# Kernel optimization log

Measured on AMD Instinct MI355X. Metric: run time of the kernel, lower is better.

## Reference

```python
import jax, jax.numpy as jnp
import numpy as np

BETA = 0.25
NUM_CODES = 512      # K
CODE_DIM = 64        # D (codebook_size)
N_TOKENS = 131072    # N


def setup_inputs() -> dict:
    key = jax.random.key(0)
    kx, kc = jax.random.split(key)
    x = jax.random.normal(kx, (N_TOKENS, CODE_DIM), dtype=jnp.float32)
    # keras 'random_uniform' initializer: U(-0.05, 0.05)
    codebook = jax.random.uniform(kc, (NUM_CODES, CODE_DIM), dtype=jnp.float32,
                                  minval=-0.05, maxval=0.05)
    return {"x": x, "codebook": codebook}


def reference(x, codebook):
    # Squared Euclidean distances [N, K] via expansion; argmin is identical
    # to argmin of tf.norm (sqrt is monotone).
    x2 = jnp.sum(x * x, axis=-1, keepdims=True)            # [N, 1]
    c2 = jnp.sum(codebook * codebook, axis=-1)             # [K]
    d2 = x2 - 2.0 * (x @ codebook.T) + c2[None, :]         # [N, K]
    indices = jnp.argmin(d2, axis=-1)                      # [N]
    quantized = jnp.take(codebook, indices, axis=0)        # [N, D]

    commitment_loss = jnp.mean((jax.lax.stop_gradient(quantized) - x) ** 2)
    codebook_loss = jnp.mean((quantized - jax.lax.stop_gradient(x)) ** 2)
    loss = BETA * commitment_loss + codebook_loss

    # straight-through estimator
    quantized_st = x + jax.lax.stop_gradient(quantized - x)
    return quantized_st, loss
```

## Files before the change

kernel.cpp:

```cpp
#include <hip/hip_runtime.h>

#define N_TOK 131072
#define K_CODES 512
#define DIM 64
#define MARGIN_S 1e-4f
#define LIST_CAP 30000

typedef __attribute__((ext_vector_type(8))) short bfx8;
typedef __attribute__((ext_vector_type(4))) float f32x4;
typedef __attribute__((ext_vector_type(4))) int i32x4;

__device__ __forceinline__ unsigned short f2bf_rn(float f) {
    unsigned u = __float_as_uint(f);
    unsigned r = (u + 0x7FFF + ((u >> 16) & 1)) >> 16;
    return (unsigned short)r;
}
__device__ __forceinline__ float bf2f(unsigned short h) {
    return __uint_as_float(((unsigned)h) << 16);
}

__device__ __forceinline__ float np_sumsq64(const float* v) {
    float r[8];
#pragma unroll
    for (int j = 0; j < 8; ++j) r[j] = __fmul_rn(v[j], v[j]);
#pragma unroll
    for (int i = 8; i < 64; i += 8) {
#pragma unroll
        for (int j = 0; j < 8; ++j)
            r[j] = __fadd_rn(r[j], __fmul_rn(v[i + j], v[i + j]));
    }
    return __fadd_rn(__fadd_rn(__fadd_rn(r[0], r[1]), __fadd_rn(r[2], r[3])),
                     __fadd_rn(__fadd_rn(r[4], r[5]), __fadd_rn(r[6], r[7])));
}

__global__ __launch_bounds__(256) void vq_prep(
    const float* __restrict__ cb, float* __restrict__ cnorm,
    float* __restrict__ c2h, unsigned short* __restrict__ cbh,
    unsigned short* __restrict__ cbl)
{
    int k = blockIdx.x * 256 + threadIdx.x;
    if (k >= K_CODES) return;
    float v[DIM];
#pragma unroll
    for (int d = 0; d < DIM; ++d) {
        float f = cb[k * DIM + d];
        v[d] = f;
        unsigned short h = f2bf_rn(f);
        cbh[k * DIM + d] = h;
        cbl[k * DIM + d] = f2bf_rn(__fsub_rn(f, bf2f(h)));
    }
    float c2 = np_sumsq64(v);
    cnorm[k] = c2;
    c2h[k] = __fmul_rn(0.5f, c2);
}

__global__ __attribute__((amdgpu_flat_work_group_size(256, 256),
                          amdgpu_waves_per_eu(2, 2)))
void vq_screen(
    const float* __restrict__ x, const float* __restrict__ cb,
    const unsigned short* __restrict__ cbh, const unsigned short* __restrict__ cbl,
    const float* __restrict__ c2h, float* __restrict__ out,
    double* __restrict__ loss_acc, int* __restrict__ counter,
    int* __restrict__ list, int cap)
{
    __shared__ bfx8 lds_h[128 * 8];
    __shared__ bfx8 lds_l[128 * 8];
    __shared__ float lds_c2[K_CODES];
    __shared__ double wsum[4];

    const int tid = threadIdx.x;
    const int wave = (blockIdx.x << 2) + (tid >> 6);
    const int lane = tid & 63;
    const int tokb = wave << 6;
    const int lrow = lane & 15;
    const int lgrp = lane >> 4;
    const int lcol = lrow;

    const float inf = __int_as_float(0x7f800000);

    if (tid < 128) ((float4*)lds_c2)[tid] = ((const float4*)c2h)[tid];

#define SPL(F, J, AH, AL) { unsigned short h_ = f2bf_rn(F); \
    (AH)[J] = (short)h_; (AL)[J] = (short)f2bf_rn(__fsub_rn(F, bf2f(h_))); }
#define LOADX(m) \
    bfx8 ah0_##m, al0_##m, ah1_##m, al1_##m; \
    { const float* xr = x + ((size_t)(tokb + (m) * 16 + lrow) << 6) + (lgrp << 3); \
      float4 f0 = *(const float4*)xr; \
      float4 f1 = *(const float4*)(xr + 4); \
      float4 f2 = *(const float4*)(xr + 32); \
      float4 f3 = *(const float4*)(xr + 36); \
      SPL(f0.x, 0, ah0_##m, al0_##m) SPL(f0.y, 1, ah0_##m, al0_##m) \
      SPL(f0.z, 2, ah0_##m, al0_##m) SPL(f0.w, 3, ah0_##m, al0_##m) \
      SPL(f1.x, 4, ah0_##m, al0_##m) SPL(f1.y, 5, ah0_##m, al0_##m) \
      SPL(f1.z, 6, ah0_##m, al0_##m) SPL(f1.w, 7, ah0_##m, al0_##m) \
      SPL(f2.x, 0, ah1_##m, al1_##m) SPL(f2.y, 1, ah1_##m, al1_##m) \
      SPL(f2.z, 2, ah1_##m, al1_##m) SPL(f2.w, 3, ah1_##m, al1_##m) \
      SPL(f3.x, 4, ah1_##m, al1_##m) SPL(f3.y, 5, ah1_##m, al1_##m) \
      SPL(f3.z, 6, ah1_##m, al1_##m) SPL(f3.w, 7, ah1_##m, al1_##m) }
    LOADX(0) LOADX(1) LOADX(2) LOADX(3)
#undef LOADX
#undef SPL

    f32x4 best0 = {inf, inf, inf, inf}, best1 = best0, best2 = best0, best3 = best0;
    f32x4 sec0 = best0, sec1 = best0, sec2 = best0, sec3 = best0;
    i32x4 idx0 = {0, 0, 0, 0}, idx1 = idx0, idx2 = idx0, idx3 = idx0;

    for (int ph = 0; ph < 4; ++ph) {
        __syncthreads();
        {
            const bfx8* gh = (const bfx8*)cbh + (ph << 10);
            const bfx8* gl = (const bfx8*)cbl + (ph << 10);
#pragma unroll
            for (int it = 0; it < 4; ++it) {
                int g = (it << 8) + tid;
                int code = g >> 3, slot = g & 7;
                int dst = (code << 3) + (slot ^ (code & 7));
                lds_h[dst] = gh[g];
                lds_l[dst] = gl[g];
            }
        }
        __syncthreads();

        int lr_c = lrow;
        int s0_c = lgrp ^ (lr_c & 7);
        bfx8 bh0 = lds_h[(lr_c << 3) + s0_c];
        bfx8 bh1 = lds_h[(lr_c << 3) + (s0_c ^ 4)];
        bfx8 bl0 = lds_l[(lr_c << 3) + s0_c];
        bfx8 bl1 = lds_l[(lr_c << 3) + (s0_c ^ 4)];
        float cn = lds_c2[(ph << 7) + lr_c];

#pragma unroll
        for (int ctl = 0; ctl < 8; ++ctl) {
            const int code = (ph << 7) + (ctl << 4) + lrow;
            bfx8 nh0 = bh0, nh1 = bh1, nl0 = bl0, nl1 = bl1;
            float cnn = cn;
            if (ctl < 7) {
                int lr_n = ((ctl + 1) << 4) + lrow;
                int s0_n = lgrp ^ (lr_n & 7);
                nh0 = lds_h[(lr_n << 3) + s0_n];
                nh1 = lds_h[(lr_n << 3) + (s0_n ^ 4)];
                nl0 = lds_l[(lr_n << 3) + s0_n];
                nl1 = lds_l[(lr_n << 3) + (s0_n ^ 4)];
                cnn = lds_c2[(ph << 7) + lr_n];
            }

#define MACC(m) \
            f32x4 accP##m = {0.f, 0.f, 0.f, 0.f}; \
            f32x4 accQ##m = {0.f, 0.f, 0.f, 0.f}; \
            accP##m = __builtin_amdgcn_mfma_f32_16x16x32_bf16(ah0_##m, bh0, accP##m, 0, 0, 0); \
            accQ##m = __builtin_amdgcn_mfma_f32_16x16x32_bf16(ah1_##m, bh1, accQ##m, 0, 0, 0); \
            accP##m = __builtin_amdgcn_mfma_f32_16x16x32_bf16(al0_##m, bh0, accP##m, 0, 0, 0); \
            accQ##m = __builtin_amdgcn_mfma_f32_16x16x32_bf16(al1_##m, bh1, accQ##m, 0, 0, 0); \
            accP##m = __builtin_amdgcn_mfma_f32_16x16x32_bf16(ah0_##m, bl0, accP##m, 0, 0, 0); \
            accQ##m = __builtin_amdgcn_mfma_f32_16x16x32_bf16(ah1_##m, bl1, accQ##m, 0, 0, 0);
            MACC(0) MACC(1) MACC(2) MACC(3)
#undef MACC

#define UPD1(m, R) { float s = cn - (accP##m[R] + accQ##m[R]); \
            bool p = s < best##m[R]; \
            sec##m[R] = p ? best##m[R] : fminf(sec##m[R], s); \
            best##m[R] = p ? s : best##m[R]; \
            idx##m[R] = p ? code : idx##m[R]; }
#define UPDM(m) UPD1(m, 0) UPD1(m, 1) UPD1(m, 2) UPD1(m, 3)
            UPDM(0) UPDM(1) UPDM(2) UPDM(3)
#undef UPDM
#undef UPD1

            bh0 = nh0; bh1 = nh1; bl0 = nl0; bl1 = nl1; cn = cnn;
        }
    }

    i32x4 pk0, pk1, pk2, pk3;
#define REDR(m, R) { float b = best##m[R], sc = sec##m[R]; int ix = idx##m[R]; \
    _Pragma("unroll") \
    for (int off = 1; off < 16; off <<= 1) { \
        float ob = __shfl_xor(b, off, 64); \
        float os = __shfl_xor(sc, off, 64); \
        int   oi = __shfl_xor(ix, off, 64); \
        bool take = (ob < b) || (ob == b && oi < ix); \
        float ns = take ? fminf(b, os) : fminf(sc, ob); \
        b = take ? ob : b; ix = take ? oi : ix; sc = ns; } \
    pk##m[R] = ix | (((sc - b) < MARGIN_S) ? (1 << 30) : 0); }
#define REDM(m) REDR(m, 0) REDR(m, 1) REDR(m, 2) REDR(m, 3)
    REDM(0) REDM(1) REDM(2) REDM(3)
#undef REDM
#undef REDR

    double ls = 0.0;
#define EPI1(m, R) { int fi = pk##m[R]; \
    int bidx_t = fi & 0xFFFF; \
    int t = tokb + (m) * 16 + (lgrp << 2) + (R); \
    float4 xv = *((const float4*)(x + ((size_t)t << 6)) + lcol); \
    float4 qv = *((const float4*)(cb + ((size_t)bidx_t << 6)) + lcol); \
    float4 ov; \
    float e0 = __fsub_rn(qv.x, xv.x); ov.x = __fadd_rn(xv.x, e0); \
    float e1 = __fsub_rn(qv.y, xv.y); ov.y = __fadd_rn(xv.y, e1); \
    float e2 = __fsub_rn(qv.z, xv.z); ov.z = __fadd_rn(xv.z, e2); \
    float e3 = __fsub_rn(qv.w, xv.w); ov.w = __fadd_rn(xv.w, e3); \
    *((float4*)(out + ((size_t)t << 6)) + lcol) = ov; \
    if (!(fi >> 30)) \
        ls += (double)e0 * e0 + (double)e1 * e1 + (double)e2 * e2 + (double)e3 * e3; \
    else if (lcol == 0) { int pos = atomicAdd(counter, 1); \
                          if (pos < cap) list[pos] = t; } }
#define EPIM(m) EPI1(m, 0) EPI1(m, 1) EPI1(m, 2) EPI1(m, 3)
    EPIM(0) EPIM(1) EPIM(2) EPIM(3)
#undef EPIM
#undef EPI1

#pragma unroll
    for (int off = 32; off > 0; off >>= 1) ls += __shfl_down(ls, off, 64);
    if (lane == 0) wsum[tid >> 6] = ls;
    __syncthreads();
    if (tid == 0)
        atomicAdd(loss_acc, (wsum[0] + wsum[1]) + (wsum[2] + wsum[3]));
}

__global__ __launch_bounds__(256) void vq_rerank(
    const float* __restrict__ x, const float* __restrict__ cb,
    const float* __restrict__ cnorm, float* __restrict__ out,
    double* __restrict__ loss_acc, const int* __restrict__ counter,
    const int* __restrict__ list, int cap)
{
    int cnt = *counter; if (cnt > cap) cnt = cap;
    const int lane = threadIdx.x & 63;
    const int wid = (blockIdx.x << 2) + (threadIdx.x >> 6);
    const int nw = gridDim.x << 2;
    double ls = 0.0;

    for (int i = wid; i < cnt; i += nw) {
        const int t = list[i];
        float xr[DIM];
        {
            const float4* xv = (const float4*)(x + ((size_t)t << 6));
#pragma unroll
            for (int q = 0; q < 16; ++q) {
                float4 v = xv[q];
                xr[4 * q + 0] = v.x; xr[4 * q + 1] = v.y;
                xr[4 * q + 2] = v.z; xr[4 * q + 3] = v.w;
            }
        }
        const float x2 = np_sumsq64(xr);
        float best = __int_as_float(0x7f800000);
        int bi = 0;
#pragma unroll 2
        for (int j = 0; j < 8; ++j) {
            const int k = (j << 6) + lane;
            const float4* c = (const float4*)(cb + ((size_t)k << 6));
            float a = 0.f;
#pragma unroll
            for (int q = 0; q < 16; ++q) {
                float4 f = c[q];
                a = __fmaf_rn(xr[4 * q + 0], f.x, a);
                a = __fmaf_rn(xr[4 * q + 1], f.y, a);
                a = __fmaf_rn(xr[4 * q + 2], f.z, a);
                a = __fmaf_rn(xr[4 * q + 3], f.w, a);
            }
            float d2 = __fadd_rn(__fsub_rn(x2, __fmul_rn(2.0f, a)), cnorm[k]);
            bool p = d2 < best;
            best = p ? d2 : best; bi = p ? k : bi;
        }
#pragma unroll
        for (int off = 1; off < 64; off <<= 1) {
            float ob = __shfl_xor(best, off, 64);
            int   oi = __shfl_xor(bi, off, 64);
            bool take = (ob < best) || (ob == best && oi < bi);
            best = take ? ob : best; bi = take ? oi : bi;
        }
        float xv = x[((size_t)t << 6) + lane];
        float q  = cb[((size_t)bi << 6) + lane];
        float e = __fsub_rn(q, xv);
        out[((size_t)t << 6) + lane] = __fadd_rn(xv, e);
        ls += (double)e * (double)e;
    }
#pragma unroll
    for (int off = 32; off > 0; off >>= 1) ls += __shfl_down(ls, off, 64);
    if (lane == 0 && ls != 0.0) atomicAdd(loss_acc, ls);
}

__global__ void vq_final(const double* __restrict__ loss_acc,
                         float* __restrict__ out_loss)
{
    if (threadIdx.x == 0 && blockIdx.x == 0) {
        double mean = *loss_acc / (double)((size_t)N_TOK * DIM);
        *out_loss = (float)(1.25 * mean);
    }
}

extern "C" void kernel_launch(void* const* d_in, const int* in_sizes, int n_in,
                              void* d_out, int out_size, void* d_ws, size_t ws_size,
                              hipStream_t stream) {
    const float* x  = (const float*)d_in[0];
    const float* cb = (const float*)d_in[1];
    float* out = (float*)d_out;
    float* out_loss = out + (size_t)N_TOK * DIM;

    char* ws = (char*)d_ws;
    double* loss_acc = (double*)ws;
    int* counter = (int*)(ws + 8);
    float* cnorm = (float*)(ws + 64);
    float* c2h = (float*)(ws + 2112);
    unsigned short* cbh = (unsigned short*)(ws + 4608);
    unsigned short* cbl = (unsigned short*)(ws + 70144);
    int* list = (int*)(ws + 135680);

    hipMemsetAsync(d_ws, 0, 16, stream);
    vq_prep<<<2, 256, 0, stream>>>(cb, cnorm, c2h, cbh, cbl);
    vq_screen<<<N_TOK / 256, 256, 0, stream>>>(x, cb, cbh, cbl, c2h, out,
                                               loss_acc, counter, list, LIST_CAP);
    vq_rerank<<<256, 256, 0, stream>>>(x, cb, cnorm, out, loss_acc,
                                       counter, list, LIST_CAP);
    vq_final<<<1, 64, 0, stream>>>(loss_acc, out_loss);
}
```

Baseline: 84.71 us.

## Fuse ambiguous-token rerank into screen kernel, drop global list and atomics

Instead of appending ambiguous tokens to a global list via atomics and reranking them in a separate kernel, each wave now reranks its own flagged tokens right after the epilogue. It does this with a ballot loop, staging the token's x row in reused LDS and computing exact fp32 distances to all 512 codes with eight independent accumulators. This removes a kernel launch, the list atomics and the list traffic. Per-thread loss accumulation also moves from double to float, which is cheaper but slightly less precise. The cost is wave divergence and tail imbalance when some waves hold many ambiguous tokens, plus extra register pressure in the screen kernel.

```diff
diff --git a/kernel.cpp b/kernel.cpp
--- a/kernel.cpp
+++ b/kernel.cpp
@@ -4,7 +4,7 @@
 #define K_CODES 512
 #define DIM 64
 #define MARGIN_S 1e-4f
-#define LIST_CAP 30000
+#define INF_F __int_as_float(0x7f800000)
 
 typedef __attribute__((ext_vector_type(8))) short bfx8;
 typedef __attribute__((ext_vector_type(4))) float f32x4;
@@ -54,14 +54,59 @@
     c2h[k] = __fmul_rn(0.5f, c2);
 }
 
+__device__ __forceinline__ void rerank_token(
+    int t, const float* __restrict__ x, const float* __restrict__ cb,
+    const float* __restrict__ cnorm, float* __restrict__ out,
+    float* lds_xw, int lane, float& ls)
+{
+    lds_xw[lane] = x[((size_t)t << 6) + lane];
+    const float x2 = np_sumsq64(lds_xw);
+
+    float a0 = 0.f, a1 = 0.f, a2 = 0.f, a3 = 0.f,
+          a4 = 0.f, a5 = 0.f, a6 = 0.f, a7 = 0.f;
+#pragma unroll
+    for (int q = 0; q < 16; ++q) {
+        float4 xq = ((const float4*)lds_xw)[q];
+#define DOT(J, A) { \
+        float4 cv = *(const float4*)(cb + ((size_t)(((J) << 6) + lane) << 6) + (q << 2)); \
+        A = __fmaf_rn(xq.x, cv.x, A); \
+        A = __fmaf_rn(xq.y, cv.y, A); \
+        A = __fmaf_rn(xq.z, cv.z, A); \
+        A = __fmaf_rn(xq.w, cv.w, A); }
+        DOT(0, a0) DOT(1, a1) DOT(2, a2) DOT(3, a3)
+        DOT(4, a4) DOT(5, a5) DOT(6, a6) DOT(7, a7)
+#undef DOT
+    }
+
+    float best = INF_F;
+    int bi = 0;
+#define SEL(J, A) { \
+    float d2 = __fadd_rn(__fsub_rn(x2, __fmul_rn(2.0f, A)), cnorm[((J) << 6) + lane]); \
+    bool p = d2 < best; best = p ? d2 : best; bi = p ? ((J) << 6) + lane : bi; }
+    SEL(0, a0) SEL(1, a1) SEL(2, a2) SEL(3, a3)
+    SEL(4, a4) SEL(5, a5) SEL(6, a6) SEL(7, a7)
+#undef SEL
+#pragma unroll
+    for (int off = 1; off < 64; off <<= 1) {
+        float ob = __shfl_xor(best, off, 64);
+        int   oi = __shfl_xor(bi, off, 64);
+        bool take = (ob < best) || (ob == best && oi < bi);
+        best = take ? ob : best; bi = take ? oi : bi;
+    }
+    float xv = x[((size_t)t << 6) + lane];
+    float q  = cb[((size_t)bi << 6) + lane];
+    float e = __fsub_rn(q, xv);
+    out[((size_t)t << 6) + lane] = __fadd_rn(xv, e);
+    ls += e * e;
+}
+
 __global__ __attribute__((amdgpu_flat_work_group_size(256, 256),
                           amdgpu_waves_per_eu(2, 2)))
 void vq_screen(
     const float* __restrict__ x, const float* __restrict__ cb,
     const unsigned short* __restrict__ cbh, const unsigned short* __restrict__ cbl,
-    const float* __restrict__ c2h, float* __restrict__ out,
-    double* __restrict__ loss_acc, int* __restrict__ counter,
-    int* __restrict__ list, int cap)
+    const float* __restrict__ c2h, const float* __restrict__ cnorm,
+    float* __restrict__ out, double* __restrict__ loss_acc)
 {
     __shared__ bfx8 lds_h[128 * 8];
     __shared__ bfx8 lds_l[128 * 8];
@@ -76,7 +121,7 @@
     const int lgrp = lane >> 4;
     const int lcol = lrow;
 
-    const float inf = __int_as_float(0x7f800000);
+    const float inf = INF_F;
 
     if (tid < 128) ((float4*)lds_c2)[tid] = ((const float4*)c2h)[tid];
 
@@ -170,6 +215,9 @@
         }
     }
 
+    __syncthreads();
+    float* lds_xw = ((float*)lds_h) + ((tid >> 6) << 6);
+
     i32x4 pk0, pk1, pk2, pk3;
 #define REDR(m, R) { float b = best##m[R], sc = sec##m[R]; int ix = idx##m[R]; \
     _Pragma("unroll") \
@@ -186,7 +234,7 @@
 #undef REDM
 #undef REDR
 
-    double ls = 0.0;
+    float ls = 0.f;
 #define EPI1(m, R) { int fi = pk##m[R]; \
     int bidx_t = fi & 0xFFFF; \
     int t = tokb + (m) * 16 + (lgrp << 2) + (R); \
@@ -199,82 +247,30 @@
     float e3 = __fsub_rn(qv.w, xv.w); ov.w = __fadd_rn(xv.w, e3); \
     *((float4*)(out + ((size_t)t << 6)) + lcol) = ov; \
     if (!(fi >> 30)) \
-        ls += (double)e0 * e0 + (double)e1 * e1 + (double)e2 * e2 + (double)e3 * e3; \
-    else if (lcol == 0) { int pos = atomicAdd(counter, 1); \
-                          if (pos < cap) list[pos] = t; } }
+        ls += e0 * e0 + e1 * e1 + e2 * e2 + e3 * e3; }
 #define EPIM(m) EPI1(m, 0) EPI1(m, 1) EPI1(m, 2) EPI1(m, 3)
     EPIM(0) EPIM(1) EPIM(2) EPIM(3)
 #undef EPIM
 #undef EPI1
 
+#define RER(m, R) { int fi = pk##m[R]; \
+    unsigned long long msk = __ballot((fi >> 30) && lrow == 0); \
+    while (msk) { \
+        int b = __ffsll((long long)msk) - 1; msk &= msk - 1; \
+        int t = tokb + (m) * 16 + ((b >> 4) << 2) + (R); \
+        rerank_token(t, x, cb, cnorm, out, lds_xw, lane, ls); } }
+    RER(0, 0) RER(0, 1) RER(0, 2) RER(0, 3)
+    RER(1, 0) RER(1, 1) RER(1, 2) RER(1, 3)
+    RER(2, 0) RER(2, 1) RER(2, 2) RER(2, 3)
+    RER(3, 0) RER(3, 1) RER(3, 2) RER(3, 3)
+#undef RER
+
 #pragma unroll
     for (int off = 32; off > 0; off >>= 1) ls += __shfl_down(ls, off, 64);
-    if (lane == 0) wsum[tid >> 6] = ls;
+    if (lane == 0) wsum[tid >> 6] = (double)ls;
     __syncthreads();
     if (tid == 0)
         atomicAdd(loss_acc, (wsum[0] + wsum[1]) + (wsum[2] + wsum[3]));
-}
-
-__global__ __launch_bounds__(256) void vq_rerank(
-    const float* __restrict__ x, const float* __restrict__ cb,
-    const float* __restrict__ cnorm, float* __restrict__ out,
-    double* __restrict__ loss_acc, const int* __restrict__ counter,
-    const int* __restrict__ list, int cap)
-{
-    int cnt = *counter; if (cnt > cap) cnt = cap;
-    const int lane = threadIdx.x & 63;
-    const int wid = (blockIdx.x << 2) + (threadIdx.x >> 6);
-    const int nw = gridDim.x << 2;
-    double ls = 0.0;
-
-    for (int i = wid; i < cnt; i += nw) {
-        const int t = list[i];
-        float xr[DIM];
-        {
-            const float4* xv = (const float4*)(x + ((size_t)t << 6));
-#pragma unroll
-            for (int q = 0; q < 16; ++q) {
-                float4 v = xv[q];
-                xr[4 * q + 0] = v.x; xr[4 * q + 1] = v.y;
-                xr[4 * q + 2] = v.z; xr[4 * q + 3] = v.w;
-            }
-        }
-        const float x2 = np_sumsq64(xr);
-        float best = __int_as_float(0x7f800000);
-        int bi = 0;
-#pragma unroll 2
-        for (int j = 0; j < 8; ++j) {
-            const int k = (j << 6) + lane;
-            const float4* c = (const float4*)(cb + ((size_t)k << 6));
-            float a = 0.f;
-#pragma unroll
-            for (int q = 0; q < 16; ++q) {
-                float4 f = c[q];
-                a = __fmaf_rn(xr[4 * q + 0], f.x, a);
-                a = __fmaf_rn(xr[4 * q + 1], f.y, a);
-                a = __fmaf_rn(xr[4 * q + 2], f.z, a);
-                a = __fmaf_rn(xr[4 * q + 3], f.w, a);
-            }
-            float d2 = __fadd_rn(__fsub_rn(x2, __fmul_rn(2.0f, a)), cnorm[k]);
-            bool p = d2 < best;
-            best = p ? d2 : best; bi = p ? k : bi;
-        }
-#pragma unroll
-        for (int off = 1; off < 64; off <<= 1) {
-            float ob = __shfl_xor(best, off, 64);
-            int   oi = __shfl_xor(bi, off, 64);
-            bool take = (ob < best) || (ob == best && oi < bi);
-            best = take ? ob : best; bi = take ? oi : bi;
-        }
-        float xv = x[((size_t)t << 6) + lane];
-        float q  = cb[((size_t)bi << 6) + lane];
-        float e = __fsub_rn(q, xv);
-        out[((size_t)t << 6) + lane] = __fadd_rn(xv, e);
-        ls += (double)e * (double)e;
-    }
-#pragma unroll
-    for (int off = 32; off > 0; off >>= 1) ls += __shfl_down(ls, off, 64);
-    if (lane == 0 && ls != 0.0) atomicAdd(loss_acc, ls);
 }
 
 __global__ void vq_final(const double* __restrict__ loss_acc,
@@ -296,18 +292,14 @@
 
     char* ws = (char*)d_ws;
     double* loss_acc = (double*)ws;
-    int* counter = (int*)(ws + 8);
     float* cnorm = (float*)(ws + 64);
     float* c2h = (float*)(ws + 2112);
     unsigned short* cbh = (unsigned short*)(ws + 4608);
     unsigned short* cbl = (unsigned short*)(ws + 70144);
-    int* list = (int*)(ws + 135680);
 
     hipMemsetAsync(d_ws, 0, 16, stream);
     vq_prep<<<2, 256, 0, stream>>>(cb, cnorm, c2h, cbh, cbl);
-    vq_screen<<<N_TOK / 256, 256, 0, stream>>>(x, cb, cbh, cbl, c2h, out,
-                                               loss_acc, counter, list, LIST_CAP);
-    vq_rerank<<<256, 256, 0, stream>>>(x, cb, cnorm, out, loss_acc,
-                                       counter, list, LIST_CAP);
+    vq_screen<<<N_TOK / 256, 256, 0, stream>>>(x, cb, cbh, cbl, c2h, cnorm,
+                                               out, loss_acc);
     vq_final<<<1, 64, 0, stream>>>(loss_acc, out_loss);
 }
```

Measured after the change: 133.9 us. +58.1%, slower.
